# Optimization experiments

Hardware: AMD Instinct MI355X
Metric: run time of the kernel (lower is better)

Reference implementation:

```python
import jax, jax.numpy as jnp
import numpy as np

C = 384       # in_channels
P = 64        # patch_size (H = W = P)
NH = 3        # num_heads
EPS = 1e-5
SCALE = (C // NH) ** -0.5  # head_dim in torch code = in_channels // num_heads


def _ln(x, w, b):
    m = jnp.mean(x, axis=-1, keepdims=True)
    v = jnp.var(x, axis=-1, keepdims=True)
    return (x - m) / jnp.sqrt(v + EPS) * w + b


def _dwt2d(x):
    # Haar DWT, x: [B, C, H, W] -> [B, 4C, H/2, W/2] channels = [LL, HL, LH, HH]
    x01 = x[:, :, 0::2, :] / 2
    x02 = x[:, :, 1::2, :] / 2
    x1 = x01[:, :, :, 0::2]
    x2 = x02[:, :, :, 0::2]
    x3 = x01[:, :, :, 1::2]
    x4 = x02[:, :, :, 1::2]
    return jnp.concatenate(
        [x1 + x2 + x3 + x4, -x1 - x2 + x3 + x4, -x1 + x2 - x3 + x4, x1 - x2 - x3 + x4],
        axis=1)


def _iwt2d(x):
    # inverse Haar, x: [B, 4C, h, w] -> [B, C, 2h, 2w]
    B, C4, h, w = x.shape
    c = C4 // 4
    x1 = x[:, 0:c] / 2
    x2 = x[:, c:2 * c] / 2
    x3 = x[:, 2 * c:3 * c] / 2
    x4 = x[:, 3 * c:4 * c] / 2
    out = jnp.zeros((B, c, h * 2, w * 2), x.dtype)
    out = out.at[:, :, 0::2, 0::2].set(x1 - x2 - x3 + x4)
    out = out.at[:, :, 1::2, 0::2].set(x1 - x2 + x3 - x4)
    out = out.at[:, :, 0::2, 1::2].set(x1 + x2 - x3 - x4)
    out = out.at[:, :, 1::2, 1::2].set(x1 + x2 + x3 + x4)
    return out


def setup_inputs():
    key = jax.random.key(0)
    ks = jax.random.split(key, 6)
    B, L = 8, P * P
    s = 0.02
    f32 = jnp.float32
    return {
        "sf": jax.random.normal(ks[0], (B, L, C), f32),
        "wf": jax.random.normal(ks[1], (B, L, C), f32),
        "q_w": jax.random.normal(ks[2], (C, C), f32) * s,
        "q_b": jnp.zeros((C,), f32),
        "q_ln_w": jnp.ones((C,), f32),
        "q_ln_b": jnp.zeros((C,), f32),
        "kv_w": jax.random.normal(ks[3], (2 * C, C), f32) * s,
        "kv_b": jnp.zeros((2 * C,), f32),
        "kv_ln_w": jnp.ones((2 * C,), f32),
        "kv_ln_b": jnp.zeros((2 * C,), f32),
        "out_w": jax.random.normal(ks[4], (C, C), f32) * s,
        "out_b": jnp.zeros((C,), f32),
    }


def reference(sf, wf, q_w, q_b, q_ln_w, q_ln_b, kv_w, kv_b, kv_ln_w, kv_ln_b, out_w, out_b):
    B, L, _ = sf.shape
    H = W = P
    h, w = H // 2, W // 2
    n = h * w  # L // 4

    t_sf = _ln(sf @ q_w.T + q_b, q_ln_w, q_ln_b)            # [B, L, C]
    t_wf = _ln(wf @ kv_w.T + kv_b, kv_ln_w, kv_ln_b)        # [B, L, 2C]

    t_sf = t_sf.reshape(B, H, W, C).transpose(0, 3, 1, 2)
    t_wf = t_wf.reshape(B, H, W, 2 * C).transpose(0, 3, 1, 2)

    t_sf = _dwt2d(t_sf).transpose(0, 2, 3, 1).reshape(B, n, 4 * C)
    t_wf = _dwt2d(t_wf).transpose(0, 2, 3, 1).reshape(B, n, 8 * C)

    k_all, v_all = jnp.split(t_wf, 2, axis=-1)              # each [B, n, 4C]
    q1, q2 = t_sf[..., :C], t_sf[..., C:]
    k1, k2 = k_all[..., :C], k_all[..., C:]
    v1, v2 = v_all[..., :C], v_all[..., C:]

    # branch 1: full single-head attention on LL sub-band (no scale, as in source)
    att1 = jax.nn.softmax(jnp.einsum('bnc,bmc->bnm', q1, k1), axis=-1)
    x1 = jnp.einsum('bnm,bmc->bnc', att1, v1)
    x1 = x1.reshape(B, h, w, C).transpose(0, 3, 1, 2)       # [B, C, h, w]

    # branch 2: multi-head attention on high-freq sub-bands, per-head dim = 3C/NH = C
    d = (3 * C) // NH
    q2 = q2.reshape(B, n, NH, d).transpose(0, 2, 1, 3)      # [B, NH, n, d]
    k2 = k2.reshape(B, n, NH, d).transpose(0, 2, 1, 3)
    v2 = v2.reshape(B, n, NH, d).transpose(0, 2, 3, 1)      # [B, NH, d, n]
    att2 = jax.nn.softmax(jnp.einsum('bhnd,bhmd->bhnm', q2, k2) * SCALE, axis=-1)
    x2 = jnp.einsum('bhdm,bhmn->bhdn', v2, att2)            # [B, NH, d, n]
    x2 = x2.reshape(B, NH * d, h, w)                        # [B, 3C, h, w]

    x = jnp.concatenate([x1, x2], axis=1)                   # [B, 4C, h, w]
    x = _iwt2d(x)                                           # [B, C, H, W]
    x = x.transpose(0, 2, 3, 1).reshape(B, L, C)
    return x @ out_w.T + out_b
```

## Files before the change

kernel.cpp:

```cpp
#include <hip/hip_runtime.h>
#include <hip/hip_bf16.h>

typedef unsigned short u16;
typedef unsigned int u32;
typedef __attribute__((ext_vector_type(8))) short short8;
typedef __attribute__((ext_vector_type(4))) float f32x4;

#define MFMA_BF16(A, B, C) __builtin_amdgcn_mfma_f32_16x16x32_bf16(A, B, C, 0, 0, 0)

#define SCALE2 0.08838834764831845f
#define LNEPS 1e-5f

__device__ __forceinline__ float b2f(u16 u) {
  return __uint_as_float(((u32)u) << 16);
}
__device__ __forceinline__ u16 f2b(float f) {
  u32 x = __float_as_uint(f);
  return (u16)((x + 0x7fffu + ((x >> 16) & 1u)) >> 16);
}
__device__ __forceinline__ float ldf(const float* p) { return *p; }
__device__ __forceinline__ float ldf(const u16* p) { return b2f(*p); }
__device__ __forceinline__ void stf(float* p, float v) { *p = v; }
__device__ __forceinline__ void stf(u16* p, float v) { *p = f2b(v); }

template <int SPLIT, typename TX, typename TO>
__global__ __launch_bounds__(256) void gemm_mfma(
    const TX* __restrict__ X, const float* __restrict__ W,
    const float* __restrict__ bias, TO* __restrict__ out) {
  __shared__ __align__(16) u16 AH[128 * 40];
  __shared__ __align__(16) u16 BH[128 * 40];
  __shared__ __align__(16) u16 AL[SPLIT ? 128 * 40 : 8];
  __shared__ __align__(16) u16 BL[SPLIT ? 128 * 40 : 8];
  const int tid = threadIdx.x;
  const int w = tid >> 6, lane = tid & 63;
  const int t = lane & 15, qd = lane >> 4;
  const int wm = w & 1, wn = w >> 1;
  const int m0 = blockIdx.y * 128, n0 = blockIdx.x * 128;
  f32x4 acc[4][4];
#pragma unroll
  for (int i = 0; i < 4; ++i)
#pragma unroll
    for (int j = 0; j < 4; ++j) acc[i][j] = (f32x4){0.f, 0.f, 0.f, 0.f};
  for (int kt = 0; kt < 384; kt += 32) {
#pragma unroll
    for (int rep = 0; rep < 4; ++rep) {
      int e = tid + rep * 256;
      int m = e >> 3, k4 = (e & 7) * 4;
      if constexpr (sizeof(TX) == 4) {
        float4 v = *(const float4*)(X + (size_t)(m0 + m) * 384 + kt + k4);
        u16 h0 = f2b(v.x), h1 = f2b(v.y), h2 = f2b(v.z), h3 = f2b(v.w);
        u32 hp0 = (u32)h0 | ((u32)h1 << 16), hp1 = (u32)h2 | ((u32)h3 << 16);
        *(uint2*)&AH[m * 40 + k4] = make_uint2(hp0, hp1);
        if (SPLIT) {
          u16 l0 = f2b(v.x - b2f(h0)), l1 = f2b(v.y - b2f(h1));
          u16 l2 = f2b(v.z - b2f(h2)), l3 = f2b(v.w - b2f(h3));
          *(uint2*)&AL[m * 40 + k4] =
              make_uint2((u32)l0 | ((u32)l1 << 16), (u32)l2 | ((u32)l3 << 16));
        }
      } else {
        uint2 raw = *(const uint2*)(X + (size_t)(m0 + m) * 384 + kt + k4);
        *(uint2*)&AH[m * 40 + k4] = raw;
      }
      float4 wv = *(const float4*)(W + (size_t)(n0 + m) * 384 + kt + k4);
      u16 wh0 = f2b(wv.x), wh1 = f2b(wv.y), wh2 = f2b(wv.z), wh3 = f2b(wv.w);
      *(uint2*)&BH[m * 40 + k4] =
          make_uint2((u32)wh0 | ((u32)wh1 << 16), (u32)wh2 | ((u32)wh3 << 16));
      if (SPLIT) {
        u16 wl0 = f2b(wv.x - b2f(wh0)), wl1 = f2b(wv.y - b2f(wh1));
        u16 wl2 = f2b(wv.z - b2f(wh2)), wl3 = f2b(wv.w - b2f(wh3));
        *(uint2*)&BL[m * 40 + k4] =
            make_uint2((u32)wl0 | ((u32)wl1 << 16), (u32)wl2 | ((u32)wl3 << 16));
      }
    }
    __syncthreads();
    short8 af[4], bf[4], al[4], bl[4];
#pragma unroll
    for (int mi = 0; mi < 4; ++mi) {
      af[mi] = *(const short8*)&AH[(wm * 64 + mi * 16 + t) * 40 + qd * 8];
      bf[mi] = *(const short8*)&BH[(wn * 64 + mi * 16 + t) * 40 + qd * 8];
      if (SPLIT) {
        al[mi] = *(const short8*)&AL[(wm * 64 + mi * 16 + t) * 40 + qd * 8];
        bl[mi] = *(const short8*)&BL[(wn * 64 + mi * 16 + t) * 40 + qd * 8];
      }
    }
#pragma unroll
    for (int mi = 0; mi < 4; ++mi)
#pragma unroll
      for (int ni = 0; ni < 4; ++ni) {
        acc[mi][ni] = MFMA_BF16(af[mi], bf[ni], acc[mi][ni]);
        if (SPLIT) {
          acc[mi][ni] = MFMA_BF16(al[mi], bf[ni], acc[mi][ni]);
          acc[mi][ni] = MFMA_BF16(af[mi], bl[ni], acc[mi][ni]);
        }
      }
    __syncthreads();
  }
#pragma unroll
  for (int ni = 0; ni < 4; ++ni) {
    int n = n0 + wn * 64 + ni * 16 + t;
    float bv = bias[n];
#pragma unroll
    for (int mi = 0; mi < 4; ++mi)
#pragma unroll
      for (int r = 0; r < 4; ++r) {
        int m = m0 + wm * 64 + mi * 16 + qd * 4 + r;
        stf(&out[(size_t)m * 384 + n], acc[mi][ni][r] + bv);
      }
  }
}

template <typename T>
__global__ __launch_bounds__(256) void ln_inplace(
    T* __restrict__ Tb, const float* __restrict__ w, const float* __restrict__ b, int N) {
  const int row = blockIdx.x, tid = threadIdx.x;
  T* Tr = Tb + (size_t)row * N;
  float vals[3];
  float s = 0.f, ss = 0.f;
  int nv = 0;
  for (int i = tid; i < N; i += 256) {
    float v = ldf(&Tr[i]);
    vals[nv++] = v;
    s += v; ss += v * v;
  }
#pragma unroll
  for (int mk = 32; mk; mk >>= 1) { s += __shfl_xor(s, mk); ss += __shfl_xor(ss, mk); }
  __shared__ float red[8];
  if ((tid & 63) == 0) { red[tid >> 6] = s; red[4 + (tid >> 6)] = ss; }
  __syncthreads();
  s = red[0] + red[1] + red[2] + red[3];
  ss = red[4] + red[5] + red[6] + red[7];
  float inv = 1.f / (float)N;
  float mean = s * inv;
  float var = fmaxf(ss * inv - mean * mean, 0.f);
  float rstd = rsqrtf(var + LNEPS);
  nv = 0;
  for (int i = tid; i < N; i += 256) {
    float v = (vals[nv++] - mean) * rstd * w[i] + b[i];
    stf(&Tr[i], v);
  }
}

__global__ __launch_bounds__(256) void ln_wf_split(
    float* __restrict__ lo, u16* __restrict__ hi,
    const float* __restrict__ w, const float* __restrict__ b) {
  const int row = blockIdx.x, tid = threadIdx.x;
  float* L = lo + (size_t)row * 384;
  u16* H = hi + (size_t)row * 384;
  float vals[3];
  float s = 0.f, ss = 0.f;
  int nv = 0;
  for (int i = tid; i < 768; i += 256) {
    float v = (i < 384) ? L[i] : b2f(H[i - 384]);
    vals[nv++] = v;
    s += v; ss += v * v;
  }
#pragma unroll
  for (int mk = 32; mk; mk >>= 1) { s += __shfl_xor(s, mk); ss += __shfl_xor(ss, mk); }
  __shared__ float red[8];
  if ((tid & 63) == 0) { red[tid >> 6] = s; red[4 + (tid >> 6)] = ss; }
  __syncthreads();
  s = red[0] + red[1] + red[2] + red[3];
  ss = red[4] + red[5] + red[6] + red[7];
  float mean = s * (1.f / 768.f);
  float var = fmaxf(ss * (1.f / 768.f) - mean * mean, 0.f);
  float rstd = rsqrtf(var + LNEPS);
  nv = 0;
  for (int i = tid; i < 768; i += 256) {
    float v = (vals[nv++] - mean) * rstd * w[i] + b[i];
    if (i < 384) L[i] = v; else H[i - 384] = f2b(v);
  }
}

__global__ __launch_bounds__(256) void dwt_sf(
    const float* __restrict__ T, u16* __restrict__ q1h, u16* __restrict__ q1l,
    u16* __restrict__ q2) {
  const int blk = blockIdx.x;
  const int b = blk >> 10, pos = blk & 1023;
  const int i = pos >> 5, j = pos & 31;
  const int p00 = (i * 2) * 64 + j * 2;
  const float* base = T + (size_t)b * 4096 * 384;
  for (int ch = threadIdx.x; ch < 384; ch += 256) {
    float a  = base[(size_t)p00 * 384 + ch];
    float cc = base[(size_t)(p00 + 1) * 384 + ch];
    float bb = base[(size_t)(p00 + 64) * 384 + ch];
    float dd = base[(size_t)(p00 + 65) * 384 + ch];
    float s0 = 0.5f * ( a + bb + cc + dd);
    float s1 = 0.5f * (-a - bb + cc + dd);
    float s2 = 0.5f * (-a + bb - cc + dd);
    float s3 = 0.5f * ( a - bb - cc + dd);
    size_t po = (size_t)(b * 1024 + pos) * 384 + ch;
    u16 h = f2b(s0);
    q1h[po] = h;
    q1l[po] = f2b(s0 - b2f(h));
    q2[(size_t)((b * 3 + 0) * 1024 + pos) * 384 + ch] = f2b(s1);
    q2[(size_t)((b * 3 + 1) * 1024 + pos) * 384 + ch] = f2b(s2);
    q2[(size_t)((b * 3 + 2) * 1024 + pos) * 384 + ch] = f2b(s3);
  }
}

__global__ __launch_bounds__(256) void dwt_wf_split(
    const float* __restrict__ lo, const u16* __restrict__ hi,
    u16* __restrict__ k1h, u16* __restrict__ k1l, u16* __restrict__ v1,
    u16* __restrict__ k2, u16* __restrict__ v2) {
  const int blk = blockIdx.x;
  const int b = blk >> 10, pos = blk & 1023;
  const int i = pos >> 5, j = pos & 31;
  const int p00 = (i * 2) * 64 + j * 2;
  for (int ch = threadIdx.x; ch < 768; ch += 256) {
    float a, bb, cc, dd;
    if (ch < 384) {
      const float* base = lo + (size_t)b * 4096 * 384;
      a  = base[(size_t)p00 * 384 + ch];
      cc = base[(size_t)(p00 + 1) * 384 + ch];
      bb = base[(size_t)(p00 + 64) * 384 + ch];
      dd = base[(size_t)(p00 + 65) * 384 + ch];
    } else {
      const u16* base = hi + (size_t)b * 4096 * 384;
      int c = ch - 384;
      a  = b2f(base[(size_t)p00 * 384 + c]);
      cc = b2f(base[(size_t)(p00 + 1) * 384 + c]);
      bb = b2f(base[(size_t)(p00 + 64) * 384 + c]);
      dd = b2f(base[(size_t)(p00 + 65) * 384 + c]);
    }
    float s0 = 0.5f * ( a + bb + cc + dd);
    float s1 = 0.5f * (-a - bb + cc + dd);
    float s2 = 0.5f * (-a + bb - cc + dd);
    float s3 = 0.5f * ( a - bb - cc + dd);
    if (ch < 384) {
      size_t po = (size_t)(b * 1024 + pos) * 384 + ch;
      u16 h = f2b(s0);
      k1h[po] = h;
      k1l[po] = f2b(s0 - b2f(h));
      v1[po] = f2b(s2);
      k2[(size_t)((b * 3 + 1) * 1024 + pos) * 384 + ch] = f2b(s1);
      v2[(size_t)((b * 3 + 1) * 1024 + pos) * 384 + ch] = f2b(s3);
    } else {
      int c = ch - 384;
      k2[(size_t)((b * 3 + 0) * 1024 + pos) * 384 + c] = f2b(s0);
      k2[(size_t)((b * 3 + 2) * 1024 + pos) * 384 + c] = f2b(s1);
      v2[(size_t)((b * 3 + 0) * 1024 + pos) * 384 + c] = f2b(s2);
      v2[(size_t)((b * 3 + 2) * 1024 + pos) * 384 + c] = f2b(s3);
    }
  }
}

__global__ __launch_bounds__(256) void transpose_rm(
    const u16* __restrict__ in, u16* __restrict__ out) {
  __shared__ u16 T[64][65];
  const int tid = threadIdx.x;
  const int bh = blockIdx.z, r0 = blockIdx.y * 64, c0 = blockIdx.x * 64;
  const u16* ip = in + ((size_t)bh * 1024 + r0) * 384 + c0;
  for (int i = tid; i < 2048; i += 256) {
    int r = i >> 5, c2 = i & 31;
    u32 v = *(const u32*)(ip + (size_t)r * 384 + c2 * 2);
    T[c2 * 2][r] = (u16)v;
    T[c2 * 2 + 1][r] = (u16)(v >> 16);
  }
  __syncthreads();
  u16* op = out + ((size_t)bh * 384 + c0) * 1024 + r0;
  for (int i = tid; i < 2048; i += 256) {
    int c = i >> 5, r2 = i & 31;
    u32 v = (u32)T[c][r2 * 2] | ((u32)T[c][r2 * 2 + 1] << 16);
    *(u32*)(op + (size_t)c * 1024 + r2 * 2) = v;
  }
}

__device__ __forceinline__ void xcd8(int L, int& bh, int& o0) {
  bh = L & 7;
  o0 = (L >> 3) * 16;
}
__device__ __forceinline__ void xcd24v2(int L, int& bh, int& o0) {
  int s = L >> 3;
  bh = (s >> 4) * 8 + (L & 7);
  o0 = (s & 15) * 64;
}

__global__ __launch_bounds__(256) void att2_stats(
    const u16* __restrict__ q, const u16* __restrict__ k,
    float2* __restrict__ stats, float scale) {
  __shared__ __align__(16) u16 S[2][12 * 32 * 40];
  const int tid = threadIdx.x, w = tid >> 6, lane = tid & 63;
  const int t = lane & 15, qd = lane >> 4;
  int bh, o0;
  xcd24v2(blockIdx.x, bh, o0);
  short8 Ah[12];
  {
    const u16* qp = q + ((size_t)bh * 1024 + o0 + w * 16 + t) * 384 + qd * 8;
#pragma unroll
    for (int ks = 0; ks < 12; ++ks) Ah[ks] = *(const short8*)(qp + ks * 32);
  }
  float m[4] = {-1e30f, -1e30f, -1e30f, -1e30f}, l[4] = {0.f, 0.f, 0.f, 0.f};
  const u16* kb = k + (size_t)bh * 1024 * 384;
  int buf = 0;
  for (int st = 0; st < 32; ++st) {
#pragma unroll
    for (int i = 0; i < 6; ++i) {
      int u = tid + i * 256;
      int r = u / 48, c8 = u % 48;
      int ks = c8 >> 2, qq = c8 & 3;
      uint4 v = *(const uint4*)(kb + (size_t)(st * 32 + r) * 384 + c8 * 8);
      *(uint4*)&S[buf][(ks * 32 + r) * 40 + qq * 8] = v;
    }
    __syncthreads();
    f32x4 Sa0 = {0.f,0.f,0.f,0.f}, Sb0 = {0.f,0.f,0.f,0.f};
    f32x4 Sa1 = {0.f,0.f,0.f,0.f}, Sb1 = {0.f,0.f,0.f,0.f};
#pragma unroll
    for (int ks = 0; ks < 12; ks += 2) {
      short8 B00 = *(const short8*)&S[buf][(ks * 32 + t) * 40 + qd * 8];
      short8 B01 = *(const short8*)&S[buf][((ks + 1) * 32 + t) * 40 + qd * 8];
      short8 B10 = *(const short8*)&S[buf][(ks * 32 + 16 + t) * 40 + qd * 8];
      short8 B11 = *(const short8*)&S[buf][((ks + 1) * 32 + 16 + t) * 40 + qd * 8];
      Sa0 = MFMA_BF16(Ah[ks], B00, Sa0);
      Sb0 = MFMA_BF16(Ah[ks + 1], B01, Sb0);
      Sa1 = MFMA_BF16(Ah[ks], B10, Sa1);
      Sb1 = MFMA_BF16(Ah[ks + 1], B11, Sb1);
    }
#pragma unroll
    for (int r = 0; r < 4; ++r) {
      float s0 = (Sa0[r] + Sb0[r]) * scale;
      float s1 = (Sa1[r] + Sb1[r]) * scale;
      float mx = fmaxf(s0, s1);
#pragma unroll
      for (int mk = 1; mk < 16; mk <<= 1) mx = fmaxf(mx, __shfl_xor(mx, mk));
      float nm = fmaxf(m[r], mx);
      float e = __expf(s0 - nm) + __expf(s1 - nm);
#pragma unroll
      for (int mk = 1; mk < 16; mk <<= 1) e += __shfl_xor(e, mk);
      l[r] = l[r] * __expf(m[r] - nm) + e;
      m[r] = nm;
    }
    buf ^= 1;
  }
  if (t == 0) {
#pragma unroll
    for (int r = 0; r < 4; ++r)
      stats[(size_t)bh * 1024 + o0 + w * 16 + qd * 4 + r] =
          make_float2(m[r], 1.f / l[r]);
  }
}

__global__ __launch_bounds__(256, 2) void att2_accum(
    const u16* __restrict__ own, const u16* __restrict__ str,
    const u16* __restrict__ vt, const float2* __restrict__ stats,
    u16* __restrict__ xall, float scale) {
  __shared__ __align__(16) u16 SQ[12 * 32 * 40];
  __shared__ __align__(16) u16 SV[24 * 16 * 40];
  __shared__ __align__(16) u16 P[4][16 * 40];
  const int tid = threadIdx.x, w = tid >> 6, lane = tid & 63;
  const int t = lane & 15, qd = lane >> 4;
  int bh, o0;
  xcd24v2(blockIdx.x, bh, o0);
  short8 Ah[12];
  {
    const u16* op = own + ((size_t)bh * 1024 + o0 + w * 16 + t) * 384 + qd * 8;
#pragma unroll
    for (int ks = 0; ks < 12; ++ks) Ah[ks] = *(const short8*)(op + ks * 32);
  }
  f32x4 acc[24];
#pragma unroll
  for (int i = 0; i < 24; ++i) acc[i] = (f32x4){0.f, 0.f, 0.f, 0.f};
  const u16* sb = str + (size_t)bh * 1024 * 384;
  const u16* vb = vt + (size_t)bh * 384 * 1024;
  u16* Pw = &P[w][0];
  for (int st = 0; st < 32; ++st) {
    __syncthreads();
#pragma unroll
    for (int i = 0; i < 6; ++i) {
      int u = tid + i * 256;
      int r = u / 48, c8 = u % 48;
      int ks = c8 >> 2, qq = c8 & 3;
      uint4 v = *(const uint4*)(sb + (size_t)(st * 32 + r) * 384 + c8 * 8);
      *(uint4*)&SQ[(ks * 32 + r) * 40 + qq * 8] = v;
    }
#pragma unroll
    for (int i = 0; i < 6; ++i) {
      int u = tid + i * 256;
      int d = u >> 2, cq = u & 3;
      uint4 v = *(const uint4*)(vb + (size_t)d * 1024 + st * 32 + cq * 8);
      *(uint4*)&SV[d * 40 + cq * 8] = v;
    }
    float2 cs0 = stats[(size_t)bh * 1024 + st * 32 + t];
    float2 cs1 = stats[(size_t)bh * 1024 + st * 32 + 16 + t];
    __syncthreads();
    f32x4 Sa0 = {0.f,0.f,0.f,0.f}, Sb0 = {0.f,0.f,0.f,0.f};
    f32x4 Sa1 = {0.f,0.f,0.f,0.f}, Sb1 = {0.f,0.f,0.f,0.f};
#pragma unroll
    for (int ks = 0; ks < 12; ks += 2) {
      short8 B00 = *(const short8*)&SQ[(ks * 32 + t) * 40 + qd * 8];
      short8 B01 = *(const short8*)&SQ[((ks + 1) * 32 + t) * 40 + qd * 8];
      short8 B10 = *(const short8*)&SQ[(ks * 32 + 16 + t) * 40 + qd * 8];
      short8 B11 = *(const short8*)&SQ[((ks + 1) * 32 + 16 + t) * 40 + qd * 8];
      Sa0 = MFMA_BF16(Ah[ks], B00, Sa0);
      Sb0 = MFMA_BF16(Ah[ks + 1], B01, Sb0);
      Sa1 = MFMA_BF16(Ah[ks], B10, Sa1);
      Sb1 = MFMA_BF16(Ah[ks + 1], B11, Sb1);
    }
#pragma unroll
    for (int r = 0; r < 4; ++r) {
      float p0 = __expf((Sa0[r] + Sb0[r]) * scale - cs0.x) * cs0.y;
      float p1 = __expf((Sa1[r] + Sb1[r]) * scale - cs1.x) * cs1.y;
      Pw[(qd * 4 + r) * 40 + t] = f2b(p0);
      Pw[(qd * 4 + r) * 40 + 16 + t] = f2b(p1);
    }
    short8 Pa = *(const short8*)&Pw[t * 40 + qd * 8];
#pragma unroll
    for (int nj = 0; nj < 24; ++nj) {
      short8 Vf = *(const short8*)&SV[(nj * 16 + t) * 40 + qd * 8];
      acc[nj] = MFMA_BF16(Pa, Vf, acc[nj]);
    }
  }
  const int b_out = bh / 3, off = (1 + bh % 3) * 384;
#pragma unroll
  for (int nj = 0; nj < 24; ++nj)
#pragma unroll
    for (int r = 0; r < 4; ++r) {
      int row = o0 + w * 16 + qd * 4 + r;
      int d = nj * 16 + t;
      xall[((size_t)b_out * 1024 + row) * 1536 + off + d] = f2b(acc[nj][r]);
    }
}

__global__ __launch_bounds__(256) void att1_stats(
    const u16* __restrict__ qh, const u16* __restrict__ ql,
    const u16* __restrict__ kh, const u16* __restrict__ kl,
    float2* __restrict__ stats) {
  __shared__ float Sp[2][2][16][17];
  __shared__ float2 comb[2][16];
  const int tid = threadIdx.x, w = tid >> 6, lane = tid & 63;
  const int t = lane & 15, qd = lane >> 4;
  int bh, o0;
  xcd8(blockIdx.x, bh, o0);
  const int ss = w & 1;
  const bool scorer = (w < 2);
  short8 Ah[12], R2[12];
  {
    const u16* qp = qh + ((size_t)bh * 1024 + o0 + t) * 384 + qd * 8;
#pragma unroll
    for (int ks = 0; ks < 12; ++ks) Ah[ks] = *(const short8*)(qp + ks * 32);
    if (scorer) {
      const u16* qp2 = ql + ((size_t)bh * 1024 + o0 + t) * 384 + qd * 8;
#pragma unroll
      for (int ks = 0; ks < 12; ++ks) R2[ks] = *(const short8*)(qp2 + ks * 32);
    }
  }
  float m[4] = {-1e30f, -1e30f, -1e30f, -1e30f}, l[4] = {0.f, 0.f, 0.f, 0.f};
  for (int st = 0; st < 32; ++st) {
    const int pb = st & 1;
    f32x4 S0 = {0.f, 0.f, 0.f, 0.f}, S1 = {0.f, 0.f, 0.f, 0.f};
    if (scorer) {
      const u16* kp = kh + ((size_t)bh * 1024 + st * 32 + w * 16 + t) * 384 + qd * 8;
#pragma unroll
      for (int ks = 0; ks < 12; ++ks) {
        short8 Bh = *(const short8*)(kp + ks * 32);
        S0 = MFMA_BF16(Ah[ks], Bh, S0);
        S1 = MFMA_BF16(R2[ks], Bh, S1);
      }
    } else {
      const u16* kp = kl + ((size_t)bh * 1024 + st * 32 + ss * 16 + t) * 384 + qd * 8;
#pragma unroll
      for (int ks = 0; ks < 12; ++ks) R2[ks] = *(const short8*)(kp + ks * 32);
#pragma unroll
      for (int ks = 0; ks < 12; ks += 2) {
        S0 = MFMA_BF16(Ah[ks], R2[ks], S0);
        S1 = MFMA_BF16(Ah[ks + 1], R2[ks + 1], S1);
      }
#pragma unroll
      for (int r = 0; r < 4; ++r) Sp[pb][ss][qd * 4 + r][t] = S0[r] + S1[r];
    }
    __syncthreads();
    if (scorer) {
#pragma unroll
      for (int r = 0; r < 4; ++r) {
        float s = S0[r] + S1[r] + Sp[pb][w][qd * 4 + r][t];
        float mx = s;
#pragma unroll
        for (int mk = 1; mk < 16; mk <<= 1) mx = fmaxf(mx, __shfl_xor(mx, mk));
        float nm = fmaxf(m[r], mx);
        float e = __expf(s - nm);
#pragma unroll
        for (int mk = 1; mk < 16; mk <<= 1) e += __shfl_xor(e, mk);
        l[r] = l[r] * __expf(m[r] - nm) + e;
        m[r] = nm;
      }
    }
  }
  if (scorer && t == 0) {
#pragma unroll
    for (int r = 0; r < 4; ++r) comb[w][qd * 4 + r] = make_float2(m[r], l[r]);
  }
  __syncthreads();
  if (tid < 16) {
    float2 a = comb[0][tid], b = comb[1][tid];
    float nm = fmaxf(a.x, b.x);
    float ll = a.y * __expf(a.x - nm) + b.y * __expf(b.x - nm);
    stats[(size_t)bh * 1024 + o0 + tid] = make_float2(nm, 1.f / ll);
  }
}

__global__ __launch_bounds__(256) void att1_accum(
    const u16* __restrict__ qh, const u16* __restrict__ ql,
    const u16* __restrict__ kh, const u16* __restrict__ kl,
    const u16* __restrict__ vt, const float2* __restrict__ stats,
    u16* __restrict__ xall) {
  __shared__ float Sp[2][2][16][17];
  __shared__ __align__(16) u16 P[2][16 * 40];
  const int tid = threadIdx.x, w = tid >> 6, lane = tid & 63;
  const int t = lane & 15, qd = lane >> 4;
  int bh, o0;
  xcd8(blockIdx.x, bh, o0);
  const int ss = w & 1;
  const bool scorer = (w < 2);
  short8 Ah[12], R2[12];
  float sm[4], sr[4];
  {
    const u16* qp = qh + ((size_t)bh * 1024 + o0 + t) * 384 + qd * 8;
#pragma unroll
    for (int ks = 0; ks < 12; ++ks) Ah[ks] = *(const short8*)(qp + ks * 32);
    if (scorer) {
      const u16* qp2 = ql + ((size_t)bh * 1024 + o0 + t) * 384 + qd * 8;
#pragma unroll
      for (int ks = 0; ks < 12; ++ks) R2[ks] = *(const short8*)(qp2 + ks * 32);
#pragma unroll
      for (int r = 0; r < 4; ++r) {
        float2 s2 = stats[(size_t)bh * 1024 + o0 + qd * 4 + r];
        sm[r] = s2.x; sr[r] = s2.y;
      }
    }
  }
  f32x4 acc[6];
#pragma unroll
  for (int i = 0; i < 6; ++i) acc[i] = (f32x4){0.f, 0.f, 0.f, 0.f};
  const u16* vbase = vt + ((size_t)bh * 384 + w * 96 + t) * 1024;
  for (int st = 0; st < 32; ++st) {
    const int pb = st & 1;
    f32x4 S0 = {0.f, 0.f, 0.f, 0.f}, S1 = {0.f, 0.f, 0.f, 0.f};
    if (scorer) {
      const u16* kp = kh + ((size_t)bh * 1024 + st * 32 + w * 16 + t) * 384 + qd * 8;
#pragma unroll
      for (int ks = 0; ks < 12; ++ks) {
        short8 Bh = *(const short8*)(kp + ks * 32);
        S0 = MFMA_BF16(Ah[ks], Bh, S0);
        S1 = MFMA_BF16(R2[ks], Bh, S1);
      }
    } else {
      const u16* kp = kl + ((size_t)bh * 1024 + st * 32 + ss * 16 + t) * 384 + qd * 8;
#pragma unroll
      for (int ks = 0; ks < 12; ++ks) R2[ks] = *(const short8*)(kp + ks * 32);
#pragma unroll
      for (int ks = 0; ks < 12; ks += 2) {
        S0 = MFMA_BF16(Ah[ks], R2[ks], S0);
        S1 = MFMA_BF16(Ah[ks + 1], R2[ks + 1], S1);
      }
#pragma unroll
      for (int r = 0; r < 4; ++r) Sp[pb][ss][qd * 4 + r][t] = S0[r] + S1[r];
    }
    short8 Vr[6];
#pragma unroll
    for (int nj = 0; nj < 6; ++nj)
      Vr[nj] = *(const short8*)(vbase + (size_t)nj * 16 * 1024 + st * 32 + qd * 8);
    __syncthreads();
    if (scorer) {
#pragma unroll
      for (int r = 0; r < 4; ++r) {
        float s = S0[r] + S1[r] + Sp[pb][w][qd * 4 + r][t];
        float p = __expf(s - sm[r]) * sr[r];
        P[pb][(qd * 4 + r) * 40 + w * 16 + t] = f2b(p);
      }
    }
    __syncthreads();
    short8 Pa = *(const short8*)&P[pb][t * 40 + qd * 8];
#pragma unroll
    for (int nj = 0; nj < 6; ++nj) acc[nj] = MFMA_BF16(Pa, Vr[nj], acc[nj]);
  }
#pragma unroll
  for (int nj = 0; nj < 6; ++nj)
#pragma unroll
    for (int r = 0; r < 4; ++r) {
      int row = o0 + qd * 4 + r;
      int d = w * 96 + nj * 16 + t;
      xall[((size_t)bh * 1024 + row) * 1536 + d] = f2b(acc[nj][r]);
    }
}

__global__ __launch_bounds__(256) void iwt_y(const u16* __restrict__ xall, u16* __restrict__ y) {
  const int blk = blockIdx.x;
  const int b = blk >> 10, pos = blk & 1023;
  const int i = pos >> 5, j = pos & 31;
  const u16* xr = xall + (size_t)(b * 1024 + pos) * 1536;
  u16* yb = y + (size_t)b * 4096 * 384;
  const int p00 = (i * 2) * 64 + j * 2;
  for (int c = threadIdx.x; c < 384; c += 256) {
    float g1 = 0.5f * b2f(xr[c]);
    float g2 = 0.5f * b2f(xr[c + 384]);
    float g3 = 0.5f * b2f(xr[c + 768]);
    float g4 = 0.5f * b2f(xr[c + 1152]);
    yb[(size_t)p00 * 384 + c]        = f2b(g1 - g2 - g3 + g4);
    yb[(size_t)(p00 + 64) * 384 + c] = f2b(g1 - g2 + g3 - g4);
    yb[(size_t)(p00 + 1) * 384 + c]  = f2b(g1 + g2 - g3 - g4);
    yb[(size_t)(p00 + 65) * 384 + c] = f2b(g1 + g2 + g3 + g4);
  }
}

extern "C" void kernel_launch(void* const* d_in, const int* in_sizes, int n_in,
                              void* d_out, int out_size, void* d_ws, size_t ws_size,
                              hipStream_t stream) {
  (void)in_sizes; (void)n_in; (void)out_size; (void)ws_size;
  const float* sf      = (const float*)d_in[0];
  const float* wf      = (const float*)d_in[1];
  const float* q_w     = (const float*)d_in[2];
  const float* q_b     = (const float*)d_in[3];
  const float* q_ln_w  = (const float*)d_in[4];
  const float* q_ln_b  = (const float*)d_in[5];
  const float* kv_w    = (const float*)d_in[6];
  const float* kv_b    = (const float*)d_in[7];
  const float* kv_ln_w = (const float*)d_in[8];
  const float* kv_ln_b = (const float*)d_in[9];
  const float* out_w   = (const float*)d_in[10];
  const float* out_b   = (const float*)d_in[11];
  float* out = (float*)d_out;

  char* p = (char*)d_ws;
  float* A  = (float*)p; p += 50331648;
  float* B1 = (float*)p; p += 50331648;
  u16*   B2 = (u16*)p;   p += 25165824;
  u16* q1h = (u16*)p; p += 6291456;
  u16* q1l = (u16*)p; p += 6291456;
  u16* q2  = (u16*)p; p += 18874368;
  u16* v2  = (u16*)p; p += 18874368;
  float2* stats1 = (float2*)p; p += 65536;
  float2* stats2 = (float2*)p;
  u16* k1h = (u16*)A;
  u16* k1l = k1h + 3145728;
  u16* v1  = k1l + 3145728;
  u16* k2  = v1 + 3145728;
  u16* v1t = k2 + 9437184;
  u16* xall = (u16*)B1;
  u16* v2t = B2;
  u16* y   = B2;

  gemm_mfma<1, float, float><<<dim3(3, 256), 256, 0, stream>>>(sf, q_w, q_b, A);
  ln_inplace<float><<<32768, 256, 0, stream>>>(A, q_ln_w, q_ln_b, 384);
  gemm_mfma<1, float, float><<<dim3(3, 256), 256, 0, stream>>>(wf, kv_w, kv_b, B1);
  gemm_mfma<0, float, u16><<<dim3(3, 256), 256, 0, stream>>>(wf, kv_w + 384 * 384, kv_b + 384, B2);
  ln_wf_split<<<32768, 256, 0, stream>>>(B1, B2, kv_ln_w, kv_ln_b);

  dwt_sf<<<8192, 256, 0, stream>>>(A, q1h, q1l, q2);
  dwt_wf_split<<<8192, 256, 0, stream>>>(B1, B2, k1h, k1l, v1, k2, v2);

  transpose_rm<<<dim3(6, 16, 8), 256, 0, stream>>>(v1, v1t);
  transpose_rm<<<dim3(6, 16, 24), 256, 0, stream>>>(v2, v2t);

  att1_stats<<<512, 256, 0, stream>>>(q1h, q1l, k1h, k1l, stats1);
  att2_stats<<<384, 256, 0, stream>>>(q2, k2, stats2, SCALE2);
  att1_accum<<<512, 256, 0, stream>>>(q1h, q1l, k1h, k1l, v1t, stats1, xall);
  att2_accum<<<384, 256, 0, stream>>>(k2, q2, v2t, stats2, xall, SCALE2);

  iwt_y<<<8192, 256, 0, stream>>>(xall, y);
  gemm_mfma<0, u16, float><<<dim3(3, 256), 256, 0, stream>>>(y, out_w, out_b, out);
}
```

Baseline: 860.3 us.

## Fuse LL-band attention stats and accumulation into one online-softmax kernel

```diff
diff --git a/kernel.cpp b/kernel.cpp
--- a/kernel.cpp
+++ b/kernel.cpp
@@ -165,7 +165,7 @@
   float var = fmaxf(ss * (1.f / 768.f) - mean * mean, 0.f);
   float rstd = rsqrtf(var + LNEPS);
   nv = 0;
-  for (int i = tid; i < 768; i += 256) {
+  for (int i = 0 + tid; i < 768; i += 256) {
     float v = (vals[nv++] - mean) * rstd * w[i] + b[i];
     if (i < 384) L[i] = v; else H[i - 384] = f2b(v);
   }
@@ -265,10 +265,6 @@
   }
 }
 
-__device__ __forceinline__ void xcd8(int L, int& bh, int& o0) {
-  bh = L & 7;
-  o0 = (L >> 3) * 16;
-}
 __device__ __forceinline__ void xcd24v2(int L, int& bh, int& o0) {
   int s = L >> 3;
   bh = (s >> 4) * 8 + (L & 7);
@@ -420,166 +416,118 @@
     }
 }
 
-__global__ __launch_bounds__(256) void att1_stats(
+__global__ __launch_bounds__(256, 2) void att1_fused(
     const u16* __restrict__ qh, const u16* __restrict__ ql,
     const u16* __restrict__ kh, const u16* __restrict__ kl,
-    float2* __restrict__ stats) {
-  __shared__ float Sp[2][2][16][17];
-  __shared__ float2 comb[2][16];
+    const u16* __restrict__ vt, u16* __restrict__ xall) {
+  __shared__ __align__(16) u16 KH[12 * 32 * 40];
+  __shared__ __align__(16) u16 KL[12 * 32 * 40];
+  __shared__ __align__(16) u16 P[2][16 * 40];
+  __shared__ float2 comb[2][2][16];
   const int tid = threadIdx.x, w = tid >> 6, lane = tid & 63;
   const int t = lane & 15, qd = lane >> 4;
-  int bh, o0;
-  xcd8(blockIdx.x, bh, o0);
-  const int ss = w & 1;
-  const bool scorer = (w < 2);
-  short8 Ah[12], R2[12];
+  const int wr = w & 1, sh = w >> 1;
+  const int bh = blockIdx.x & 7, o0 = (blockIdx.x >> 3) * 32;
+  short8 Ah[12], Al[12];
   {
-    const u16* qp = qh + ((size_t)bh * 1024 + o0 + t) * 384 + qd * 8;
-#pragma unroll
-    for (int ks = 0; ks < 12; ++ks) Ah[ks] = *(const short8*)(qp + ks * 32);
-    if (scorer) {
-      const u16* qp2 = ql + ((size_t)bh * 1024 + o0 + t) * 384 + qd * 8;
-#pragma unroll
-      for (int ks = 0; ks < 12; ++ks) R2[ks] = *(const short8*)(qp2 + ks * 32);
-    }
-  }
+    const u16* qp  = qh + ((size_t)bh * 1024 + o0 + wr * 16 + t) * 384 + qd * 8;
+    const u16* qp2 = ql + ((size_t)bh * 1024 + o0 + wr * 16 + t) * 384 + qd * 8;
+#pragma unroll
+    for (int ks = 0; ks < 12; ++ks) {
+      Ah[ks] = *(const short8*)(qp + ks * 32);
+      Al[ks] = *(const short8*)(qp2 + ks * 32);
+    }
+  }
+  f32x4 acc[12];
+#pragma unroll
+  for (int i = 0; i < 12; ++i) acc[i] = (f32x4){0.f, 0.f, 0.f, 0.f};
   float m[4] = {-1e30f, -1e30f, -1e30f, -1e30f}, l[4] = {0.f, 0.f, 0.f, 0.f};
+  const u16* khb = kh + (size_t)bh * 1024 * 384;
+  const u16* klb = kl + (size_t)bh * 1024 * 384;
+  const u16* vbase = vt + ((size_t)bh * 384 + sh * 192 + t) * 1024;
+#pragma unroll
+  for (int i = 0; i < 6; ++i) {
+    int u = tid + i * 256;
+    int r = u / 48, c8 = u % 48;
+    int ks = c8 >> 2, j8 = c8 & 3;
+    *(uint4*)&KH[(ks * 32 + r) * 40 + j8 * 8] =
+        *(const uint4*)(khb + (size_t)r * 384 + c8 * 8);
+    *(uint4*)&KL[(ks * 32 + r) * 40 + j8 * 8] =
+        *(const uint4*)(klb + (size_t)r * 384 + c8 * 8);
+  }
+  __syncthreads();
   for (int st = 0; st < 32; ++st) {
-    const int pb = st & 1;
-    f32x4 S0 = {0.f, 0.f, 0.f, 0.f}, S1 = {0.f, 0.f, 0.f, 0.f};
-    if (scorer) {
-      const u16* kp = kh + ((size_t)bh * 1024 + st * 32 + w * 16 + t) * 384 + qd * 8;
-#pragma unroll
-      for (int ks = 0; ks < 12; ++ks) {
-        short8 Bh = *(const short8*)(kp + ks * 32);
-        S0 = MFMA_BF16(Ah[ks], Bh, S0);
-        S1 = MFMA_BF16(R2[ks], Bh, S1);
+    short8 Vr[12];
+#pragma unroll
+    for (int nj = 0; nj < 12; ++nj)
+      Vr[nj] = *(const short8*)(vbase + (size_t)nj * 16 * 1024 + st * 32 + qd * 8);
+    f32x4 Shh = {0.f,0.f,0.f,0.f}, Slh = {0.f,0.f,0.f,0.f}, Shl = {0.f,0.f,0.f,0.f};
+#pragma unroll
+    for (int ks = 0; ks < 12; ++ks) {
+      short8 Bh = *(const short8*)&KH[(ks * 32 + sh * 16 + t) * 40 + qd * 8];
+      short8 Bl = *(const short8*)&KL[(ks * 32 + sh * 16 + t) * 40 + qd * 8];
+      Shh = MFMA_BF16(Ah[ks], Bh, Shh);
+      Slh = MFMA_BF16(Al[ks], Bh, Slh);
+      Shl = MFMA_BF16(Ah[ks], Bl, Shl);
+    }
+    float s[4], mx[4], e[4];
+#pragma unroll
+    for (int r = 0; r < 4; ++r) {
+      s[r] = Shh[r] + Slh[r] + Shl[r];
+      float v = s[r];
+#pragma unroll
+      for (int mk = 1; mk < 16; mk <<= 1) v = fmaxf(v, __shfl_xor(v, mk));
+      mx[r] = v;
+      float ee = __expf(s[r] - v);
+#pragma unroll
+      for (int mk = 1; mk < 16; mk <<= 1) ee += __shfl_xor(ee, mk);
+      e[r] = ee;
+    }
+    if (t == 0) {
+#pragma unroll
+      for (int r = 0; r < 4; ++r)
+        comb[wr][sh][qd * 4 + r] = make_float2(mx[r], e[r]);
+    }
+    __syncthreads();
+    if (st < 31) {
+#pragma unroll
+      for (int i = 0; i < 6; ++i) {
+        int u = tid + i * 256;
+        int r = u / 48, c8 = u % 48;
+        int ks = c8 >> 2, j8 = c8 & 3;
+        *(uint4*)&KH[(ks * 32 + r) * 40 + j8 * 8] =
+            *(const uint4*)(khb + (size_t)((st + 1) * 32 + r) * 384 + c8 * 8);
+        *(uint4*)&KL[(ks * 32 + r) * 40 + j8 * 8] =
+            *(const uint4*)(klb + (size_t)((st + 1) * 32 + r) * 384 + c8 * 8);
       }
-    } else {
-      const u16* kp = kl + ((size_t)bh * 1024 + st * 32 + ss * 16 + t) * 384 + qd * 8;
-#pragma unroll
-      for (int ks = 0; ks < 12; ++ks) R2[ks] = *(const short8*)(kp + ks * 32);
-#pragma unroll
-      for (int ks = 0; ks < 12; ks += 2) {
-        S0 = MFMA_BF16(Ah[ks], R2[ks], S0);
-        S1 = MFMA_BF16(Ah[ks + 1], R2[ks + 1], S1);
-      }
-#pragma unroll
-      for (int r = 0; r < 4; ++r) Sp[pb][ss][qd * 4 + r][t] = S0[r] + S1[r];
+    }
+#pragma unroll
+    for (int r = 0; r < 4; ++r) {
+      float2 c0 = comb[wr][0][qd * 4 + r];
+      float2 c1 = comb[wr][1][qd * 4 + r];
+      float nm = fmaxf(m[r], fmaxf(c0.x, c1.x));
+      float sc = __expf(m[r] - nm);
+      l[r] = l[r] * sc + c0.y * __expf(c0.x - nm) + c1.y * __expf(c1.x - nm);
+      m[r] = nm;
+#pragma unroll
+      for (int nj = 0; nj < 12; ++nj) acc[nj][r] *= sc;
+      P[wr][(qd * 4 + r) * 40 + sh * 16 + t] = f2b(__expf(s[r] - nm));
     }
     __syncthreads();
-    if (scorer) {
-#pragma unroll
-      for (int r = 0; r < 4; ++r) {
-        float s = S0[r] + S1[r] + Sp[pb][w][qd * 4 + r][t];
-        float mx = s;
-#pragma unroll
-        for (int mk = 1; mk < 16; mk <<= 1) mx = fmaxf(mx, __shfl_xor(mx, mk));
-        float nm = fmaxf(m[r], mx);
-        float e = __expf(s - nm);
-#pragma unroll
-        for (int mk = 1; mk < 16; mk <<= 1) e += __shfl_xor(e, mk);
-        l[r] = l[r] * __expf(m[r] - nm) + e;
-        m[r] = nm;
-      }
-    }
-  }
-  if (scorer && t == 0) {
-#pragma unroll
-    for (int r = 0; r < 4; ++r) comb[w][qd * 4 + r] = make_float2(m[r], l[r]);
-  }
-  __syncthreads();
-  if (tid < 16) {
-    float2 a = comb[0][tid], b = comb[1][tid];
-    float nm = fmaxf(a.x, b.x);
-    float ll = a.y * __expf(a.x - nm) + b.y * __expf(b.x - nm);
-    stats[(size_t)bh * 1024 + o0 + tid] = make_float2(nm, 1.f / ll);
-  }
-}
-
-__global__ __launch_bounds__(256) void att1_accum(
-    const u16* __restrict__ qh, const u16* __restrict__ ql,
-    const u16* __restrict__ kh, const u16* __restrict__ kl,
-    const u16* __restrict__ vt, const float2* __restrict__ stats,
-    u16* __restrict__ xall) {
-  __shared__ float Sp[2][2][16][17];
-  __shared__ __align__(16) u16 P[2][16 * 40];
-  const int tid = threadIdx.x, w = tid >> 6, lane = tid & 63;
-  const int t = lane & 15, qd = lane >> 4;
-  int bh, o0;
-  xcd8(blockIdx.x, bh, o0);
-  const int ss = w & 1;
-  const bool scorer = (w < 2);
-  short8 Ah[12], R2[12];
-  float sm[4], sr[4];
-  {
-    const u16* qp = qh + ((size_t)bh * 1024 + o0 + t) * 384 + qd * 8;
-#pragma unroll
-    for (int ks = 0; ks < 12; ++ks) Ah[ks] = *(const short8*)(qp + ks * 32);
-    if (scorer) {
-      const u16* qp2 = ql + ((size_t)bh * 1024 + o0 + t) * 384 + qd * 8;
-#pragma unroll
-      for (int ks = 0; ks < 12; ++ks) R2[ks] = *(const short8*)(qp2 + ks * 32);
-#pragma unroll
-      for (int r = 0; r < 4; ++r) {
-        float2 s2 = stats[(size_t)bh * 1024 + o0 + qd * 4 + r];
-        sm[r] = s2.x; sr[r] = s2.y;
-      }
-    }
-  }
-  f32x4 acc[6];
-#pragma unroll
-  for (int i = 0; i < 6; ++i) acc[i] = (f32x4){0.f, 0.f, 0.f, 0.f};
-  const u16* vbase = vt + ((size_t)bh * 384 + w * 96 + t) * 1024;
-  for (int st = 0; st < 32; ++st) {
-    const int pb = st & 1;
-    f32x4 S0 = {0.f, 0.f, 0.f, 0.f}, S1 = {0.f, 0.f, 0.f, 0.f};
-    if (scorer) {
-      const u16* kp = kh + ((size_t)bh * 1024 + st * 32 + w * 16 + t) * 384 + qd * 8;
-#pragma unroll
-      for (int ks = 0; ks < 12; ++ks) {
-        short8 Bh = *(const short8*)(kp + ks * 32);
-        S0 = MFMA_BF16(Ah[ks], Bh, S0);
-        S1 = MFMA_BF16(R2[ks], Bh, S1);
-      }
-    } else {
-      const u16* kp = kl + ((size_t)bh * 1024 + st * 32 + ss * 16 + t) * 384 + qd * 8;
-#pragma unroll
-      for (int ks = 0; ks < 12; ++ks) R2[ks] = *(const short8*)(kp + ks * 32);
-#pragma unroll
-      for (int ks = 0; ks < 12; ks += 2) {
-        S0 = MFMA_BF16(Ah[ks], R2[ks], S0);
-        S1 = MFMA_BF16(Ah[ks + 1], R2[ks + 1], S1);
-      }
-#pragma unroll
-      for (int r = 0; r < 4; ++r) Sp[pb][ss][qd * 4 + r][t] = S0[r] + S1[r];
-    }
-    short8 Vr[6];
-#pragma unroll
-    for (int nj = 0; nj < 6; ++nj)
-      Vr[nj] = *(const short8*)(vbase + (size_t)nj * 16 * 1024 + st * 32 + qd * 8);
-    __syncthreads();
-    if (scorer) {
-#pragma unroll
-      for (int r = 0; r < 4; ++r) {
-        float s = S0[r] + S1[r] + Sp[pb][w][qd * 4 + r][t];
-        float p = __expf(s - sm[r]) * sr[r];
-        P[pb][(qd * 4 + r) * 40 + w * 16 + t] = f2b(p);
-      }
-    }
-    __syncthreads();
-    short8 Pa = *(const short8*)&P[pb][t * 40 + qd * 8];
-#pragma unroll
-    for (int nj = 0; nj < 6; ++nj) acc[nj] = MFMA_BF16(Pa, Vr[nj], acc[nj]);
-  }
-#pragma unroll
-  for (int nj = 0; nj < 6; ++nj)
-#pragma unroll
-    for (int r = 0; r < 4; ++r) {
-      int row = o0 + qd * 4 + r;
-      int d = w * 96 + nj * 16 + t;
-      xall[((size_t)bh * 1024 + row) * 1536 + d] = f2b(acc[nj][r]);
-    }
+    short8 Pa = *(const short8*)&P[wr][t * 40 + qd * 8];
+#pragma unroll
+    for (int nj = 0; nj < 12; ++nj) acc[nj] = MFMA_BF16(Pa, Vr[nj], acc[nj]);
+  }
+#pragma unroll
+  for (int r = 0; r < 4; ++r) {
+    float inv = 1.f / l[r];
+    int row = o0 + wr * 16 + qd * 4 + r;
+#pragma unroll
+    for (int nj = 0; nj < 12; ++nj) {
+      int d = sh * 192 + nj * 16 + t;
+      xall[((size_t)bh * 1024 + row) * 1536 + d] = f2b(acc[nj][r] * inv);
+    }
+  }
 }
 
 __global__ __launch_bounds__(256) void iwt_y(const u16* __restrict__ xall, u16* __restrict__ y) {
@@ -629,6 +577,7 @@
   u16* v2  = (u16*)p; p += 18874368;
   float2* stats1 = (float2*)p; p += 65536;
   float2* stats2 = (float2*)p;
+  (void)stats1;
   u16* k1h = (u16*)A;
   u16* k1l = k1h + 3145728;
   u16* v1  = k1l + 3145728;
@@ -650,9 +599,8 @@
   transpose_rm<<<dim3(6, 16, 8), 256, 0, stream>>>(v1, v1t);
   transpose_rm<<<dim3(6, 16, 24), 256, 0, stream>>>(v2, v2t);
 
-  att1_stats<<<512, 256, 0, stream>>>(q1h, q1l, k1h, k1l, stats1);
   att2_stats<<<384, 256, 0, stream>>>(q2, k2, stats2, SCALE2);
-  att1_accum<<<512, 256, 0, stream>>>(q1h, q1l, k1h, k1l, v1t, stats1, xall);
+  att1_fused<<<256, 256, 0, stream>>>(q1h, q1l, k1h, k1l, v1t, xall);
   att2_accum<<<384, 256, 0, stream>>>(k2, q2, v2t, stats2, xall, SCALE2);
 
   iwt_y<<<8192, 256, 0, stream>>>(xall, y);
```

New measurement: 811.4 us. -5.7%, faster.
